# Kernel tuning notes

Hardware: AMD Instinct MI355X
Metric: run time of the kernel (lower is better)

Reference implementation:

```python
import jax, jax.numpy as jnp
import numpy as np

B, C, W, H = 2, 64, 96, 96
C8 = C // 8


def setup_inputs() -> dict:
    key = jax.random.key(0)
    ks = jax.random.split(key, 8)
    return {
        "x": jax.random.normal(ks[0], (B, C, W, H), dtype=jnp.float32),
        "Wq": jax.random.normal(ks[1], (C8, C), dtype=jnp.float32) * 0.05,
        "bq": jax.random.normal(ks[2], (C8,), dtype=jnp.float32) * 0.05,
        "Wk": jax.random.normal(ks[3], (C8, C), dtype=jnp.float32) * 0.05,
        "bk": jax.random.normal(ks[4], (C8,), dtype=jnp.float32) * 0.05,
        "Wv": jax.random.normal(ks[5], (C, C), dtype=jnp.float32) * 0.05,
        "bv": jax.random.normal(ks[6], (C,), dtype=jnp.float32) * 0.05,
        "gamma": jax.random.normal(ks[7], (1,), dtype=jnp.float32),
    }


def reference(x, Wq, bq, Wk, bk, Wv, bv, gamma):
    b, c, w, h = x.shape
    n = w * h
    xf = x.reshape(b, c, n)  # [B, C, N]
    # 1x1 convs are channel-mixing matmuls over flattened spatial dim
    q = jnp.einsum('oc,bcn->bno', Wq, xf) + bq          # [B, N, C//8] (proj_query, permuted)
    k = jnp.einsum('oc,bcn->bon', Wk, xf) + bk[:, None]  # [B, C//8, N] (proj_key)
    energy = jnp.einsum('bno,bom->bnm', q, k)            # [B, N, N]
    # torch softmax over dim=1 (the query index), NOT the usual dim=-1
    attn = jax.nn.softmax(energy, axis=1)                # [B, N, N]
    v = jnp.einsum('oc,bcn->bon', Wv, xf) + bv[:, None]  # [B, C, N]
    # bmm(V, attn.permute(0,2,1)): out[b,c,m] = sum_n V[b,c,n] * attn[b,m,n]
    out = jnp.einsum('bcn,bmn->bcm', v, attn).reshape(b, c, w, h)
    return gamma * out + x
```

## Files before the change

kernel.cpp:

```cpp
#include <hip/hip_runtime.h>
#include <math.h>

#define NN 9216
#define LOG2E 1.4426950408889634f

typedef __attribute__((ext_vector_type(8))) __bf16 bf16x8;
typedef __attribute__((ext_vector_type(16))) float f32x16;
typedef __attribute__((ext_vector_type(4))) unsigned int u32x4;

#define MFMA32(a,b,c) __builtin_amdgcn_mfma_f32_32x32x16_bf16(a,b,c,0,0,0)

#if __has_builtin(__builtin_amdgcn_exp2f)
#define EXP2(x) __builtin_amdgcn_exp2f(x)
#else
#define EXP2(x) exp2f(x)
#endif

__device__ __forceinline__ bf16x8 zero8() {
    bf16x8 z;
    #pragma unroll
    for (int i = 0; i < 8; i++) z[i] = (__bf16)0.0f;
    return z;
}

__device__ __forceinline__ unsigned int pk2(float a, float b) {
    unsigned short ua = __builtin_bit_cast(unsigned short, (__bf16)a);
    unsigned short ub = __builtin_bit_cast(unsigned short, (__bf16)b);
    return (unsigned int)ua | ((unsigned int)ub << 16);
}

__device__ __forceinline__ void plane_swap(unsigned int &a, unsigned int &b) {
    asm("v_permlane32_swap_b32 %0, %1" : "+v"(a), "+v"(b));
}

__device__ __forceinline__ void cp16(void* lds, const void* g) {
    __builtin_amdgcn_global_load_lds(
        (const __attribute__((address_space(1))) unsigned int*)g,
        (__attribute__((address_space(3))) unsigned int*)lds, 16, 0, 0);
}

#define OFF_QB 0
#define OFF_KB 294912
#define OFF_VB 589824
#define OFF_VF 2949120
#define OFF_DP 5308416
#define OFF_PARTS 5308416
#define WS_NEED 33619968ULL

__global__ __launch_bounds__(256) void qkv_kernel(
    const float* __restrict__ x,
    const float* __restrict__ Wq, const float* __restrict__ bq,
    const float* __restrict__ Wk, const float* __restrict__ bk,
    const float* __restrict__ Wv, const float* __restrict__ bv,
    __bf16* __restrict__ QB, __bf16* __restrict__ KB, __bf16* __restrict__ VB)
{
    __shared__ float wsh[1024], bsh[16];
    int tid = threadIdx.x;
    int z = blockIdx.z, b = blockIdx.y;
    if (z == 0) {
        for (int i = tid; i < 512; i += 256) { wsh[i] = Wq[i]; wsh[512+i] = Wk[i]; }
        if (tid < 8)  { bsh[tid] = bq[tid]; bsh[8+tid] = bk[tid]; }
    } else {
        for (int i = tid; i < 512; i += 256) wsh[i] = Wv[(z-1)*512 + i];
        if (tid < 8)  bsh[tid] = bv[(z-1)*8 + tid];
    }
    __syncthreads();

    int n = blockIdx.x * 256 + tid;

    float xc[64];
    #pragma unroll
    for (int c = 0; c < 64; c++) xc[c] = x[((size_t)(b*64 + c))*NN + n];

    if (z == 0) {
        float q[8], k[8];
        #pragma unroll
        for (int o = 0; o < 8; o++) { q[o] = bsh[o]; k[o] = bsh[8+o]; }
        #pragma unroll
        for (int c = 0; c < 64; c++) {
            float xv = xc[c];
            #pragma unroll
            for (int o = 0; o < 8; o++) {
                q[o] = fmaf(wsh[o*64+c], xv, q[o]);
                k[o] = fmaf(wsh[512+o*64+c], xv, k[o]);
            }
        }
        bf16x8 qv, kv;
        #pragma unroll
        for (int o = 0; o < 8; o++) {
            qv[o] = (__bf16)(q[o] * LOG2E);
            kv[o] = (__bf16)k[o];
        }
        *(bf16x8*)(QB + ((size_t)b*NN + n)*8) = qv;
        *(bf16x8*)(KB + ((size_t)b*NN + n)*8) = kv;
    } else {
        float v[8];
        #pragma unroll
        for (int o = 0; o < 8; o++) v[o] = bsh[o];
        #pragma unroll
        for (int c = 0; c < 64; c++) {
            float xv = xc[c];
            #pragma unroll
            for (int o = 0; o < 8; o++) v[o] = fmaf(wsh[o*64+c], xv, v[o]);
        }
        #pragma unroll
        for (int o = 0; o < 8; o++)
            VB[((size_t)(b*64 + (z-1)*8 + o))*NN + n] = (__bf16)v[o];
    }
}

__global__ __launch_bounds__(256) void stats_kernel(
    const __bf16* __restrict__ QB, const __bf16* __restrict__ KB,
    float* __restrict__ Dp)
{
    __shared__ float Dl[4][32];
    int tid = threadIdx.x;
    int lane = tid & 63, w = tid >> 6;
    int l31 = lane & 31, h = lane >> 5;
    int b = blockIdx.y, z = blockIdx.z;
    int n0 = blockIdx.x * 32;

    f32x16 Z16;
    #pragma unroll
    for (int r = 0; r < 16; r++) Z16[r] = 0.0f;

    bf16x8 kf = zero8();
    if (lane < 32)
        kf = *(const bf16x8*)(KB + ((size_t)b*NN + n0 + l31)*8);

    float Dacc[16];
    #pragma unroll
    for (int r = 0; r < 16; r++) Dacc[r] = 0.0f;

    const __bf16* Qb = QB + (size_t)b*NN*8;
    int mbase = z*2304 + w*576;
    for (int it = 0; it < 18; it++) {
        bf16x8 qf = zero8();
        if (lane < 32)
            qf = *(const bf16x8*)(Qb + (size_t)(mbase + it*32 + l31)*8);
        f32x16 e = MFMA32(kf, qf, Z16);
        #pragma unroll
        for (int r = 0; r < 16; r++) Dacc[r] += EXP2(e[r]);
    }
    #pragma unroll
    for (int r = 0; r < 16; r++) {
        #pragma unroll
        for (int mask = 1; mask < 32; mask <<= 1)
            Dacc[r] += __shfl_xor(Dacc[r], mask);
    }
    if (l31 == 0) {
        #pragma unroll
        for (int r = 0; r < 16; r++)
            Dl[w][(r&3) + 8*(r>>2) + 4*h] = Dacc[r];
    }
    __syncthreads();
    if (tid < 32)
        Dp[((size_t)(z*2 + b))*NN + n0 + tid] =
            Dl[0][tid] + Dl[1][tid] + Dl[2][tid] + Dl[3][tid];
}

__global__ __launch_bounds__(256) void foldvf_kernel(
    const float* __restrict__ Dp, const float* __restrict__ gamma_p,
    const __bf16* __restrict__ VB, __bf16* __restrict__ VF)
{
    __shared__ float Rl[64];
    int tid = threadIdx.x;
    int b = blockIdx.y, tg = blockIdx.x;
    int n0 = tg * 64;
    if (tid < 64) {
        float d = 0.0f;
        #pragma unroll
        for (int zz = 0; zz < 4; zz++)
            d += Dp[((size_t)(zz*2 + b))*NN + n0 + tid];
        Rl[tid] = gamma_p[0] / d;
    }
    __syncthreads();

    #pragma unroll
    for (int i = 0; i < 2; i++) {
        int p = tid + i*256;
        int chunk = p >> 6, lane = p & 63;
        int c  = (chunk & 1)*32 + (lane & 31);
        int nl = ((chunk >> 2) & 1)*32 + ((chunk >> 1) & 1)*16 + (lane >> 5)*8;
        bf16x8 v = *(const bf16x8*)(VB + ((size_t)(b*64 + c))*NN + n0 + nl);
        bf16x8 ov;
        #pragma unroll
        for (int j = 0; j < 8; j++)
            ov[j] = (__bf16)((float)v[j] * Rl[nl + j]);
        *(bf16x8*)(VF + (((size_t)(b*144 + tg))*8 + chunk)*512 + lane*8) = ov;
    }
}

__global__ __launch_bounds__(256) void init_kernel(
    const float* __restrict__ x, float* __restrict__ out)
{
    int i = blockIdx.x*256 + threadIdx.x;
    ((float4*)out)[i] = ((const float4*)x)[i];
}

__global__ __launch_bounds__(256) void pv_kernel(
    const __bf16* __restrict__ QB, const __bf16* __restrict__ KB,
    const __bf16* __restrict__ VF, float* __restrict__ out,
    __bf16* __restrict__ parts)
{
    __shared__ __bf16 vbuf[2][4096];
    __shared__ __bf16 klin[2][512];

    int tid = threadIdx.x;
    int lane = tid & 63, w = tid >> 6;
    int l31 = lane & 31, h = lane >> 5;
    int b = blockIdx.y, s = blockIdx.z;
    int mw = blockIdx.x * 128 + w * 32;

    f32x16 Z16;
    #pragma unroll
    for (int r = 0; r < 16; r++) Z16[r] = 0.0f;

    bf16x8 qf = zero8();
    if (lane < 32)
        qf = *(const bf16x8*)(QB + ((size_t)b*NN + mw + l31)*8);

    f32x16 acc[2];
    acc[0] = Z16; acc[1] = Z16;

    const __bf16* kbase = KB + ((size_t)b*NN + s*768)*8;
    const __bf16* vbase = VF + ((size_t)(b*144 + s*12))*8*512;

#define STAGE(bi, stq) do {                                                   \
    const __bf16* tile_ = vbase + (size_t)(stq)*4096;                         \
    cp16((char*)vbuf[bi] + w*1024,        tile_ + (w*64 + lane)*8);           \
    cp16((char*)vbuf[bi] + 4096 + w*1024, tile_ + (256 + w*64 + lane)*8);     \
    if (w == 0)                                                               \
        cp16((char*)klin[bi], kbase + ((size_t)(stq)*64 + lane)*8);           \
} while (0)

    STAGE(0, 0);

    for (int t = 0; t < 12; t++) {
        int bi = t & 1;
        __syncthreads();
        if (t < 11) {
            if (bi == 0) STAGE(1, t+1); else STAGE(0, t+1);
        }

        bf16x8 kfr0 = zero8(), kfr1 = zero8();
        if (lane < 32) {
            kfr0 = *(const bf16x8*)(klin[bi] + l31*8);
            kfr1 = *(const bf16x8*)(klin[bi] + (32 + l31)*8);
        }
        f32x16 e0 = MFMA32(kfr0, qf, Z16);
        f32x16 e1 = MFMA32(kfr1, qf, Z16);

        bf16x8 pa[2][2];
        #pragma unroll
        for (int nt = 0; nt < 2; nt++) {
            const f32x16& e = nt ? e1 : e0;
            float pf[16];
            #pragma unroll
            for (int r = 0; r < 16; r++) pf[r] = EXP2(e[r]);
            unsigned int u[8];
            #pragma unroll
            for (int q = 0; q < 8; q++) u[q] = pk2(pf[2*q], pf[2*q+1]);
            plane_swap(u[0], u[2]); plane_swap(u[1], u[3]);
            plane_swap(u[4], u[6]); plane_swap(u[5], u[7]);
            u32x4 t0 = {u[0], u[1], u[2], u[3]};
            u32x4 t1 = {u[4], u[5], u[6], u[7]};
            pa[nt][0] = __builtin_bit_cast(bf16x8, t0);
            pa[nt][1] = __builtin_bit_cast(bf16x8, t1);
        }

        __builtin_amdgcn_s_setprio(1);
        #pragma unroll
        for (int chunk = 0; chunk < 8; chunk++) {
            bf16x8 bfr = *(const bf16x8*)((char*)vbuf[bi] + chunk*1024 + lane*16);
            acc[chunk & 1] = MFMA32(pa[chunk >> 2][(chunk >> 1) & 1], bfr, acc[chunk & 1]);
        }
        __builtin_amdgcn_s_setprio(0);
    }

    if (parts != nullptr) {
        __bf16* pp = parts + ((size_t)(s*2 + b))*64*NN;
        #pragma unroll
        for (int ct = 0; ct < 2; ct++) {
            int c = ct*32 + l31;
            __bf16* row = pp + (size_t)c*NN + mw + 4*h;
            #pragma unroll
            for (int q = 0; q < 4; q++) {
                uint2 v2;
                v2.x = pk2(acc[ct][4*q],   acc[ct][4*q+1]);
                v2.y = pk2(acc[ct][4*q+2], acc[ct][4*q+3]);
                *(uint2*)(row + q*8) = v2;
            }
        }
    } else {
        #pragma unroll
        for (int ct = 0; ct < 2; ct++) {
            int c = ct*32 + l31;
            #pragma unroll
            for (int r = 0; r < 16; r++) {
                int m = mw + (r&3) + 8*(r>>2) + 4*h;
                atomicAdd(out + ((size_t)(b*64 + c))*NN + m, (float)acc[ct][r]);
            }
        }
    }
}

__global__ __launch_bounds__(256) void reduce_kernel(
    const float* __restrict__ x, const __bf16* __restrict__ parts,
    float* __restrict__ out)
{
    size_t f0 = ((size_t)blockIdx.x*256 + threadIdx.x) * 8;
    float o[8];
    float4 a = *(const float4*)(x + f0);
    float4 c = *(const float4*)(x + f0 + 4);
    o[0]=a.x; o[1]=a.y; o[2]=a.z; o[3]=a.w;
    o[4]=c.x; o[5]=c.y; o[6]=c.z; o[7]=c.w;
    #pragma unroll
    for (int sIdx = 0; sIdx < 12; sIdx++) {
        bf16x8 p = *(const bf16x8*)(parts + (size_t)sIdx*(128*NN) + f0);
        #pragma unroll
        for (int j = 0; j < 8; j++) o[j] += (float)p[j];
    }
    float4 r0 = make_float4(o[0],o[1],o[2],o[3]);
    float4 r1 = make_float4(o[4],o[5],o[6],o[7]);
    *(float4*)(out + f0) = r0;
    *(float4*)(out + f0 + 4) = r1;
}

extern "C" void kernel_launch(void* const* d_in, const int* in_sizes, int n_in,
                              void* d_out, int out_size, void* d_ws, size_t ws_size,
                              hipStream_t stream) {
    const float* x     = (const float*)d_in[0];
    const float* Wq    = (const float*)d_in[1];
    const float* bq    = (const float*)d_in[2];
    const float* Wk    = (const float*)d_in[3];
    const float* bk    = (const float*)d_in[4];
    const float* Wv    = (const float*)d_in[5];
    const float* bv    = (const float*)d_in[6];
    const float* gamma = (const float*)d_in[7];
    float* out = (float*)d_out;
    char* ws   = (char*)d_ws;

    __bf16* QB = (__bf16*)(ws + OFF_QB);
    __bf16* KB = (__bf16*)(ws + OFF_KB);
    __bf16* VB = (__bf16*)(ws + OFF_VB);
    __bf16* VF = (__bf16*)(ws + OFF_VF);
    float*  Dp = (float*)(ws + OFF_DP);

    qkv_kernel<<<dim3(36, 2, 9), 256, 0, stream>>>(x, Wq, bq, Wk, bk, Wv, bv, QB, KB, VB);
    stats_kernel<<<dim3(288, 2, 4), 256, 0, stream>>>(QB, KB, Dp);
    foldvf_kernel<<<dim3(144, 2), 256, 0, stream>>>(Dp, gamma, VB, VF);

    if (ws_size >= WS_NEED) {
        __bf16* parts = (__bf16*)(ws + OFF_PARTS);
        pv_kernel<<<dim3(72, 2, 12), 256, 0, stream>>>(QB, KB, VF, out, parts);
        reduce_kernel<<<dim3(576), 256, 0, stream>>>(x, parts, out);
    } else {
        init_kernel<<<dim3(1152), 256, 0, stream>>>(x, out);
        pv_kernel<<<dim3(72, 2, 12), 256, 0, stream>>>(QB, KB, VF, out, nullptr);
    }
}
```

Baseline: 100.6 us.

## Process two query tiles per wave in pv kernel and compute all V channels per thread

The pv kernel now has each wave handle 64 query positions (two 32-row tiles) instead of 32, so each staged K/V tile in LDS is reused twice and the grid is halved. The exp/pack of the second tile is interleaved with the MFMA loop of the first to overlap VALU and matrix work. Separately, the qkv kernel now computes all 64 V output channels per thread rather than 8 per block-z slice, cutting redundant x reads but using many more registers (64 accumulators plus 64 x values). This risks register spills and lower occupancy in both kernels, and fewer pv blocks means less parallelism.

```diff
diff --git a/kernel.cpp b/kernel.cpp
--- a/kernel.cpp
+++ b/kernel.cpp
@@ -54,15 +54,15 @@
     const float* __restrict__ Wv, const float* __restrict__ bv,
     __bf16* __restrict__ QB, __bf16* __restrict__ KB, __bf16* __restrict__ VB)
 {
-    __shared__ float wsh[1024], bsh[16];
+    __shared__ float wsh[4096], bsh[64];
     int tid = threadIdx.x;
     int z = blockIdx.z, b = blockIdx.y;
     if (z == 0) {
         for (int i = tid; i < 512; i += 256) { wsh[i] = Wq[i]; wsh[512+i] = Wk[i]; }
         if (tid < 8)  { bsh[tid] = bq[tid]; bsh[8+tid] = bk[tid]; }
     } else {
-        for (int i = tid; i < 512; i += 256) wsh[i] = Wv[(z-1)*512 + i];
-        if (tid < 8)  bsh[tid] = bv[(z-1)*8 + tid];
+        for (int i = tid; i < 4096; i += 256) wsh[i] = Wv[i];
+        if (tid < 64) bsh[tid] = bv[tid];
     }
     __syncthreads();
 
@@ -94,18 +94,18 @@
         *(bf16x8*)(QB + ((size_t)b*NN + n)*8) = qv;
         *(bf16x8*)(KB + ((size_t)b*NN + n)*8) = kv;
     } else {
-        float v[8];
-        #pragma unroll
-        for (int o = 0; o < 8; o++) v[o] = bsh[o];
+        float v[64];
+        #pragma unroll
+        for (int o = 0; o < 64; o++) v[o] = bsh[o];
         #pragma unroll
         for (int c = 0; c < 64; c++) {
             float xv = xc[c];
             #pragma unroll
-            for (int o = 0; o < 8; o++) v[o] = fmaf(wsh[o*64+c], xv, v[o]);
-        }
-        #pragma unroll
-        for (int o = 0; o < 8; o++)
-            VB[((size_t)(b*64 + (z-1)*8 + o))*NN + n] = (__bf16)v[o];
+            for (int o = 0; o < 64; o++) v[o] = fmaf(wsh[o*64+c], xv, v[o]);
+        }
+        #pragma unroll
+        for (int o = 0; o < 64; o++)
+            VB[((size_t)(b*64 + o))*NN + n] = (__bf16)v[o];
     }
 }
 
@@ -210,18 +210,20 @@
     int lane = tid & 63, w = tid >> 6;
     int l31 = lane & 31, h = lane >> 5;
     int b = blockIdx.y, s = blockIdx.z;
-    int mw = blockIdx.x * 128 + w * 32;
+    int mw = blockIdx.x * 256 + w * 64;
 
     f32x16 Z16;
     #pragma unroll
     for (int r = 0; r < 16; r++) Z16[r] = 0.0f;
 
-    bf16x8 qf = zero8();
-    if (lane < 32)
-        qf = *(const bf16x8*)(QB + ((size_t)b*NN + mw + l31)*8);
-
-    f32x16 acc[2];
-    acc[0] = Z16; acc[1] = Z16;
+    bf16x8 qfA = zero8(), qfB = zero8();
+    if (lane < 32) {
+        qfA = *(const bf16x8*)(QB + ((size_t)b*NN + mw + l31)*8);
+        qfB = *(const bf16x8*)(QB + ((size_t)b*NN + mw + 32 + l31)*8);
+    }
+
+    f32x16 accA[2], accB[2];
+    accA[0] = Z16; accA[1] = Z16; accB[0] = Z16; accB[1] = Z16;
 
     const __bf16* kbase = KB + ((size_t)b*NN + s*768)*8;
     const __bf16* vbase = VF + ((size_t)(b*144 + s*12))*8*512;
@@ -234,6 +236,25 @@
         cp16((char*)klin[bi], kbase + ((size_t)(stq)*64 + lane)*8);           \
 } while (0)
 
+#define PACK(e0, e1, pa) do {                                                 \
+    _Pragma("unroll")                                                         \
+    for (int nt = 0; nt < 2; nt++) {                                          \
+        const f32x16& e_ = nt ? e1 : e0;                                      \
+        float pf[16];                                                         \
+        _Pragma("unroll")                                                     \
+        for (int r = 0; r < 16; r++) pf[r] = EXP2(e_[r]);                     \
+        unsigned int u[8];                                                    \
+        _Pragma("unroll")                                                     \
+        for (int q = 0; q < 8; q++) u[q] = pk2(pf[2*q], pf[2*q+1]);           \
+        plane_swap(u[0], u[2]); plane_swap(u[1], u[3]);                       \
+        plane_swap(u[4], u[6]); plane_swap(u[5], u[7]);                       \
+        u32x4 t0 = {u[0], u[1], u[2], u[3]};                                  \
+        u32x4 t1 = {u[4], u[5], u[6], u[7]};                                  \
+        pa[nt][0] = __builtin_bit_cast(bf16x8, t0);                           \
+        pa[nt][1] = __builtin_bit_cast(bf16x8, t1);                           \
+    }                                                                         \
+} while (0)
+
     STAGE(0, 0);
 
     for (int t = 0; t < 12; t++) {
@@ -248,32 +269,31 @@
             kfr0 = *(const bf16x8*)(klin[bi] + l31*8);
             kfr1 = *(const bf16x8*)(klin[bi] + (32 + l31)*8);
         }
-        f32x16 e0 = MFMA32(kfr0, qf, Z16);
-        f32x16 e1 = MFMA32(kfr1, qf, Z16);
-
-        bf16x8 pa[2][2];
-        #pragma unroll
-        for (int nt = 0; nt < 2; nt++) {
-            const f32x16& e = nt ? e1 : e0;
-            float pf[16];
-            #pragma unroll
-            for (int r = 0; r < 16; r++) pf[r] = EXP2(e[r]);
-            unsigned int u[8];
-            #pragma unroll
-            for (int q = 0; q < 8; q++) u[q] = pk2(pf[2*q], pf[2*q+1]);
-            plane_swap(u[0], u[2]); plane_swap(u[1], u[3]);
-            plane_swap(u[4], u[6]); plane_swap(u[5], u[7]);
-            u32x4 t0 = {u[0], u[1], u[2], u[3]};
-            u32x4 t1 = {u[4], u[5], u[6], u[7]};
-            pa[nt][0] = __builtin_bit_cast(bf16x8, t0);
-            pa[nt][1] = __builtin_bit_cast(bf16x8, t1);
-        }
+
+        f32x16 eA0 = MFMA32(kfr0, qfA, Z16);
+        f32x16 eA1 = MFMA32(kfr1, qfA, Z16);
+        bf16x8 paA[2][2];
+        PACK(eA0, eA1, paA);
+
+        f32x16 eB0 = MFMA32(kfr0, qfB, Z16);
+        f32x16 eB1 = MFMA32(kfr1, qfB, Z16);
 
         __builtin_amdgcn_s_setprio(1);
         #pragma unroll
         for (int chunk = 0; chunk < 8; chunk++) {
             bf16x8 bfr = *(const bf16x8*)((char*)vbuf[bi] + chunk*1024 + lane*16);
-            acc[chunk & 1] = MFMA32(pa[chunk >> 2][(chunk >> 1) & 1], bfr, acc[chunk & 1]);
+            accA[chunk & 1] = MFMA32(paA[chunk >> 2][(chunk >> 1) & 1], bfr, accA[chunk & 1]);
+        }
+        __builtin_amdgcn_s_setprio(0);
+
+        bf16x8 paB[2][2];
+        PACK(eB0, eB1, paB);
+
+        __builtin_amdgcn_s_setprio(1);
+        #pragma unroll
+        for (int chunk = 0; chunk < 8; chunk++) {
+            bf16x8 bfr = *(const bf16x8*)((char*)vbuf[bi] + chunk*1024 + lane*16);
+            accB[chunk & 1] = MFMA32(paB[chunk >> 2][(chunk >> 1) & 1], bfr, accB[chunk & 1]);
         }
         __builtin_amdgcn_s_setprio(0);
     }
@@ -283,13 +303,17 @@
         #pragma unroll
         for (int ct = 0; ct < 2; ct++) {
             int c = ct*32 + l31;
-            __bf16* row = pp + (size_t)c*NN + mw + 4*h;
+            __bf16* rowA = pp + (size_t)c*NN + mw + 4*h;
+            __bf16* rowB = rowA + 32;
             #pragma unroll
             for (int q = 0; q < 4; q++) {
                 uint2 v2;
-                v2.x = pk2(acc[ct][4*q],   acc[ct][4*q+1]);
-                v2.y = pk2(acc[ct][4*q+2], acc[ct][4*q+3]);
-                *(uint2*)(row + q*8) = v2;
+                v2.x = pk2(accA[ct][4*q],   accA[ct][4*q+1]);
+                v2.y = pk2(accA[ct][4*q+2], accA[ct][4*q+3]);
+                *(uint2*)(rowA + q*8) = v2;
+                v2.x = pk2(accB[ct][4*q],   accB[ct][4*q+1]);
+                v2.y = pk2(accB[ct][4*q+2], accB[ct][4*q+3]);
+                *(uint2*)(rowB + q*8) = v2;
             }
         }
     } else {
@@ -299,7 +323,8 @@
             #pragma unroll
             for (int r = 0; r < 16; r++) {
                 int m = mw + (r&3) + 8*(r>>2) + 4*h;
-                atomicAdd(out + ((size_t)(b*64 + c))*NN + m, (float)acc[ct][r]);
+                atomicAdd(out + ((size_t)(b*64 + c))*NN + m,      (float)accA[ct][r]);
+                atomicAdd(out + ((size_t)(b*64 + c))*NN + m + 32, (float)accB[ct][r]);
             }
         }
     }
@@ -347,16 +372,16 @@
     __bf16* VF = (__bf16*)(ws + OFF_VF);
     float*  Dp = (float*)(ws + OFF_DP);
 
-    qkv_kernel<<<dim3(36, 2, 9), 256, 0, stream>>>(x, Wq, bq, Wk, bk, Wv, bv, QB, KB, VB);
+    qkv_kernel<<<dim3(36, 2, 2), 256, 0, stream>>>(x, Wq, bq, Wk, bk, Wv, bv, QB, KB, VB);
     stats_kernel<<<dim3(288, 2, 4), 256, 0, stream>>>(QB, KB, Dp);
     foldvf_kernel<<<dim3(144, 2), 256, 0, stream>>>(Dp, gamma, VB, VF);
 
     if (ws_size >= WS_NEED) {
         __bf16* parts = (__bf16*)(ws + OFF_PARTS);
-        pv_kernel<<<dim3(72, 2, 12), 256, 0, stream>>>(QB, KB, VF, out, parts);
+        pv_kernel<<<dim3(36, 2, 12), 256, 0, stream>>>(QB, KB, VF, out, parts);
         reduce_kernel<<<dim3(576), 256, 0, stream>>>(x, parts, out);
     } else {
         init_kernel<<<dim3(1152), 256, 0, stream>>>(x, out);
-        pv_kernel<<<dim3(72, 2, 12), 256, 0, stream>>>(QB, KB, VF, out, nullptr);
-    }
-}
+        pv_kernel<<<dim3(36, 2, 12), 256, 0, stream>>>(QB, KB, VF, out, nullptr);
+    }
+}
```

New measurement: 123.4 us. +22.7%, slower.
